# Optimization experiments

Hardware: AMD Instinct MI355X
Metric: run time of the kernel (lower is better)

Reference implementation:

```python
import jax, jax.numpy as jnp
from jax import lax
import numpy as np

ALPHA = 0.85   # TemporalSmoother alpha
EPS = 1e-5     # BatchNorm eps


def _bn(x, g, b):
    # eval-mode BatchNorm2d with running_mean=0, running_var=1 (fresh model)
    s = g / jnp.sqrt(1.0 + EPS)
    return x * s[None, :, None, None] + b[None, :, None, None]


def _conv(x, w, stride, pad):
    # x: NCHW (H=T, W=V), w: OIHW
    return lax.conv_general_dilated(x, w, window_strides=(stride, 1), padding=pad,
                                    dimension_numbers=('NCHW', 'OIHW', 'NCHW'))


def _block(x, A, gw, gb, g1, b1, tw, tb, g2, b2, rw, rb, stride):
    # residual 1x1 conv (always present: channels differ in every block)
    res = _conv(x, rw, stride, [(0, 0), (0, 0)]) + rb[None, :, None, None]
    # GraphConv: matmul(x, A.T) over joints, then 1x1 conv over channels
    h = jnp.einsum('nctv,wv->nctw', x, A)
    h = jnp.einsum('nctv,oc->notv', h, gw) + gb[None, :, None, None]
    # tcn: BN -> ReLU -> (9,1) conv stride (s,1) pad (4,0) -> BN
    h = jax.nn.relu(_bn(h, g1, b1))
    h = _conv(h, tw, stride, [(4, 4), (0, 0)]) + tb[None, :, None, None]
    h = _bn(h, g2, b2)
    return jax.nn.relu(h + res)


def _smooth(x):
    # EMA over time: s_t = a*s_{t-1} + (1-a)*x_t, s_0 = x_0 ; single lax.scan
    xt = jnp.moveaxis(x, 2, 0)  # (T, N, C, V)
    def step(s, xc):
        s = ALPHA * s + (1.0 - ALPHA) * xc
        return s, s
    _, ys = lax.scan(step, xt[0], xt[1:])
    return jnp.moveaxis(jnp.concatenate([xt[:1], ys], axis=0), 0, 2)


def setup_inputs() -> dict:
    key = jax.random.key(0)
    ks = jax.random.split(key, 12)
    N, C, T, V = 128, 2, 256, 18
    d = {}
    d['x'] = jax.random.normal(ks[0], (N, C, T, V), jnp.float32)
    d['A'] = jax.random.uniform(ks[1], (V, V), jnp.float32) / V  # normalized-ish adjacency
    d['dbn_g'] = jnp.ones((C * V,), jnp.float32)
    d['dbn_b'] = jnp.zeros((C * V,), jnp.float32)
    dims = [(2, 64), (64, 128), (128, 256)]
    for i, (ci, co) in enumerate(dims, 1):
        k = jax.random.split(ks[i + 1], 3)
        d[f'l{i}_gw'] = jax.random.normal(k[0], (co, ci), jnp.float32) * 0.1
        d[f'l{i}_gb'] = jnp.zeros((co,), jnp.float32)
        d[f'l{i}_bn1g'] = jnp.ones((co,), jnp.float32)
        d[f'l{i}_bn1b'] = jnp.zeros((co,), jnp.float32)
        d[f'l{i}_tw'] = jax.random.normal(k[1], (co, co, 9, 1), jnp.float32) * 0.05
        d[f'l{i}_tb'] = jnp.zeros((co,), jnp.float32)
        d[f'l{i}_bn2g'] = jnp.ones((co,), jnp.float32)
        d[f'l{i}_bn2b'] = jnp.zeros((co,), jnp.float32)
        d[f'l{i}_rw'] = jax.random.normal(k[2], (co, ci, 1, 1), jnp.float32) * 0.1
        d[f'l{i}_rb'] = jnp.zeros((co,), jnp.float32)
    d['fc_w'] = jax.random.normal(ks[10], (10, 256), jnp.float32) * 0.05
    d['fc_b'] = jnp.zeros((10,), jnp.float32)
    return d


def reference(x, A, dbn_g, dbn_b,
              l1_gw, l1_gb, l1_bn1g, l1_bn1b, l1_tw, l1_tb, l1_bn2g, l1_bn2b, l1_rw, l1_rb,
              l2_gw, l2_gb, l2_bn1g, l2_bn1b, l2_tw, l2_tb, l2_bn2g, l2_bn2b, l2_rw, l2_rb,
              l3_gw, l3_gb, l3_bn1g, l3_bn1b, l3_tw, l3_tb, l3_bn2g, l3_bn2b, l3_rw, l3_rb,
              fc_w, fc_b):
    N, C, T, V = x.shape
    # data_bn: BatchNorm1d over C*V features, eval mode (mean 0, var 1)
    xb = x.transpose(0, 1, 3, 2).reshape(N, C * V, T)
    s = dbn_g / jnp.sqrt(1.0 + EPS)
    xb = xb * s[None, :, None] + dbn_b[None, :, None]
    h = xb.reshape(N, C, V, T).transpose(0, 1, 3, 2)  # back to (N,C,T,V)
    h = _block(h, A, l1_gw, l1_gb, l1_bn1g, l1_bn1b, l1_tw, l1_tb, l1_bn2g, l1_bn2b, l1_rw, l1_rb, 1)
    h = _smooth(h)
    h = _block(h, A, l2_gw, l2_gb, l2_bn1g, l2_bn1b, l2_tw, l2_tb, l2_bn2g, l2_bn2b, l2_rw, l2_rb, 2)
    h = _smooth(h)
    h = _block(h, A, l3_gw, l3_gb, l3_bn1g, l3_bn1b, l3_tw, l3_tb, l3_bn2g, l3_bn2b, l3_rw, l3_rb, 2)
    h = _smooth(h)
    h = jnp.mean(h, axis=(2, 3))  # AdaptiveAvgPool2d((1,1))
    return h @ fc_w.T + fc_b
```

## Files before the change

### kernel.cpp

```cpp
#include <hip/hip_runtime.h>
#include <hip/hip_bf16.h>

#define EPS 1e-5f


typedef __attribute__((ext_vector_type(8))) short bf16x8;
typedef __attribute__((ext_vector_type(4))) float f32x4;
typedef __attribute__((ext_vector_type(4))) unsigned u32x4;

__device__ __forceinline__ unsigned short f2bf(float f) {
  unsigned u = __builtin_bit_cast(unsigned, f);
  u = (u + 0x7FFFu + ((u >> 16) & 1u)) >> 16;
  return (unsigned short)u;
}
__device__ __forceinline__ float bf2f(unsigned short h) {
  unsigned u = (unsigned)h << 16;
  return __builtin_bit_cast(float, u);
}


__global__ __launch_bounds__(256, 4) void k_transpose(
    const float* __restrict__ in, float* __restrict__ out, int rows, int cols) {
  int i = blockIdx.x * 256 + threadIdx.x;
  if (i < rows * cols) {
    int r = i / cols, c = i % cols;
    out[c * rows + r] = in[i];
  }
}

__global__ __launch_bounds__(256, 4) void k_beta(
    const float* __restrict__ bn2g, const float* __restrict__ bn2b,
    const float* __restrict__ tb, const float* __restrict__ rb,
    float* __restrict__ beta, int Co) {
  int o = blockIdx.x * 256 + threadIdx.x;
  if (o < Co)
    beta[o] = bn2g[o] * (1.0f / sqrtf(1.0f + EPS)) * tb[o] + bn2b[o] + rb[o];
}

__global__ __launch_bounds__(256, 4) void k_s1b1(
    const float* __restrict__ bn1g, const float* __restrict__ bn1b,
    const float* __restrict__ gb, float* __restrict__ s1v,
    float* __restrict__ b1p, int Co) {
  int o = blockIdx.x * 256 + threadIdx.x;
  if (o < Co) {
    float s1 = bn1g[o] * (1.0f / sqrtf(1.0f + EPS));
    s1v[o] = s1;
    b1p[o] = fmaf(s1, gb[o], bn1b[o]);
  }
}

__global__ __launch_bounds__(256, 4) void k_pack_conv9(
    const float* __restrict__ tw, const float* __restrict__ bn2g,
    unsigned short* __restrict__ out, int CO) {
  int KCc = CO / 32;
  int total = (CO / 16) * 9 * KCc * 512;
  int i = blockIdx.x * 256 + threadIdx.x;
  if (i >= total) return;
  int jj = i & 7, lane = (i >> 3) & 63, rest = i >> 9;
  int kc = rest % KCc; rest /= KCc;
  int j = rest % 9, ot = rest / 9;
  int q = lane >> 4, m = lane & 15;
  int c = kc * 32 + q * 8 + jj, o = ot * 16 + m;
  out[i] = f2bf(tw[((size_t)o * CO + c) * 9 + j] * bn2g[o] * (1.0f / sqrtf(1.0f + EPS)));
}

__global__ __launch_bounds__(256, 4) void k_pack_k32(
    const float* __restrict__ W, unsigned short* __restrict__ out, int K, int M) {
  int total = (M / 16) * (K / 32) * 512;
  int i = blockIdx.x * 256 + threadIdx.x;
  if (i >= total) return;
  int j = i & 7, lane = (i >> 3) & 63, rest = i >> 9;
  int kc = rest % (K / 32), ot = rest / (K / 32);
  int q = lane >> 4, m = lane & 15;
  int c = kc * 32 + q * 8 + j, o = ot * 16 + m;
  out[i] = f2bf(W[(size_t)o * K + c]);
}

__global__ __launch_bounds__(256, 4) void k_front1g(
    const float* __restrict__ x, const float* __restrict__ dbng,
    const float* __restrict__ dbnb, const float* __restrict__ Amat,
    const float* __restrict__ gw, const float* __restrict__ gb,
    const float* __restrict__ bn1g, const float* __restrict__ bn1b,
    unsigned short* __restrict__ Gt1, float* __restrict__ xb1) {
  int n = blockIdx.x, t0 = blockIdx.y * 64;
  __shared__ float xb[2304];
  __shared__ float xm[2304];
  __shared__ float As[324];
  __shared__ float g0s[64], g1s[64], bps[64];
  __shared__ unsigned short ldsT[64 * 65];
  const float rs = 1.0f / sqrtf(1.0f + EPS);
  for (int e = threadIdx.x; e < 324; e += 256) As[e] = Amat[e];
  if (threadIdx.x < 64) {
    int o = threadIdx.x;
    float s1 = bn1g[o] * rs;
    g0s[o] = gw[o * 2 + 0] * s1;
    g1s[o] = gw[o * 2 + 1] * s1;
    bps[o] = fmaf(s1, gb[o], bn1b[o]);
  }
  for (int e = threadIdx.x; e < 2304; e += 256) {
    int c = e / 1152, r = e % 1152;
    int v = r % 18;
    xb[e] = x[(n * 2 + c) * 4608 + t0 * 18 + r] * (dbng[c * 18 + v] * rs) + dbnb[c * 18 + v];
  }
  __syncthreads();
  for (int e = threadIdx.x; e < 2304; e += 256) {
    int c = e / 1152, r = e % 1152;
    int v = r / 64, tt = r % 64;
    xb1[((size_t)(n * 2 + c) * 18 + v) * 256 + t0 + tt] = xb[c * 1152 + tt * 18 + v];
  }
  for (int e = threadIdx.x; e < 2304; e += 256) {
    int c = e / 1152, r = e % 1152;
    int tt = r / 18, v = r % 18;
    const float* xr = &xb[c * 1152 + tt * 18];
    float z = 0.0f;
#pragma unroll
    for (int w = 0; w < 18; w++) z = fmaf(As[v * 18 + w], xr[w], z);
    xm[e] = z;
  }
  __syncthreads();
  for (int v = 0; v < 18; v++) {
    for (int e = threadIdx.x; e < 4096; e += 256) {
      int o = e >> 6, tt = e & 63;
      float z = fmaf(g0s[o], xm[tt * 18 + v], fmaf(g1s[o], xm[1152 + tt * 18 + v], bps[o]));
      z = z > 0.0f ? z : 0.0f;
      ldsT[o * 65 + tt] = f2bf(z);
    }
    __syncthreads();
    for (int e = threadIdx.x; e < 4096; e += 256) {
      int tt = e >> 6, o = e & 63;
      Gt1[((size_t)(n * 18 + v) * 272 + 8 + t0 + tt) * 64 + o] = ldsT[o * 65 + tt];
    }
    __syncthreads();
  }
  if (blockIdx.y == 0 || blockIdx.y == 3) {
    int base = (blockIdx.y == 0) ? 0 : 264;
    for (int e = threadIdx.x; e < 18 * 8 * 64; e += 256) {
      int v = e / 512, r = e % 512;
      int tg = base + (r >> 6), o = r & 63;
      Gt1[((size_t)(n * 18 + v) * 272 + tg) * 64 + o] = 0;
    }
  }
}

template <int CO, int T>
__global__ __launch_bounds__(256, 4) void k_amixX(
    const unsigned short* __restrict__ Xt, unsigned short* __restrict__ Xm,
    const float* __restrict__ Amat) {
  int idx = blockIdx.x * 256 + threadIdx.x;
  int c = idx & (CO - 1);
  int t = (idx / CO) & (T - 1);
  int n = idx / (CO * T);
  const size_t stride = (size_t)T * CO;
  const unsigned short* bp = Xt + (size_t)n * 18 * stride + (size_t)t * CO + c;
  unsigned short* op = Xm + (size_t)n * 18 * stride + (size_t)t * CO + c;
  float xs[18];
#pragma unroll
  for (int w = 0; w < 18; w++) xs[w] = bf2f(bp[w * stride]);
#pragma unroll
  for (int v = 0; v < 18; v++) {
    float z = 0.0f;
#pragma unroll
    for (int w = 0; w < 18; w++) z = fmaf(Amat[v * 18 + w], xs[w], z);
    op[v * stride] = f2bf(z);
  }
}

template <int CI, int CO, int TIN>
__global__ __launch_bounds__(64, 4) void k_ugemmG(
    const unsigned short* __restrict__ Xm, const unsigned short* __restrict__ Ag,
    const float* __restrict__ s1v, const float* __restrict__ b1p,
    unsigned short* __restrict__ Gt) {
  constexpr int NP = 18 * TIN;
  constexpr int Trr = TIN + 16;
  const int n = blockIdx.x;
  const int p0 = blockIdx.y * 32;
  const int otg = blockIdx.z;
  const int lane = threadIdx.x;
  const int q = lane >> 4, nn = lane & 15;
  constexpr int KC = CI / 32;
  const int v = p0 / TIN;
  const int tb = p0 % TIN;
  __shared__ unsigned short ldsT[32 * 36];
  f32x4 acc[2][2] = {};
  const unsigned short* Xn = Xm + (size_t)n * NP * CI;
  for (int kc = 0; kc < KC; kc++) {
    bf16x8 A[2];
#pragma unroll
    for (int i = 0; i < 2; i++)
      A[i] = *(const bf16x8*)(Ag + (((size_t)(otg * 2 + i) * KC + kc) * 64 + lane) * 8);
#pragma unroll
    for (int u = 0; u < 2; u++) {
      bf16x8 B = *(const bf16x8*)(Xn + (size_t)(p0 + u * 16 + nn) * CI + kc * 32 + q * 8);
#pragma unroll
      for (int i = 0; i < 2; i++)
        acc[i][u] = __builtin_amdgcn_mfma_f32_16x16x32_bf16(A[i], B, acc[i][u], 0, 0, 0);
    }
  }
#pragma unroll
  for (int i = 0; i < 2; i++) {
    int obl = i * 16 + q * 4;
    int ob = otg * 32 + obl;
    const float4 s4 = *(const float4*)&s1v[ob];
    const float4 b4 = *(const float4*)&b1p[ob];
#pragma unroll
    for (int u = 0; u < 2; u++) {
      unsigned short zb[4];
#pragma unroll
      for (int r = 0; r < 4; r++) {
        float z = fmaf(acc[i][u][r], ((const float*)&s4)[r], ((const float*)&b4)[r]);
        z = z > 0.0f ? z : 0.0f;
        zb[r] = f2bf(z);
      }
      *(unsigned long long*)&ldsT[(u * 16 + nn) * 36 + obl] =
          *(const unsigned long long*)zb;
    }
  }
  __syncthreads();
  for (int e = lane; e < 1024; e += 64) {
    int tq = e >> 5, cq2 = e & 31;
    Gt[((size_t)(n * 18 + v) * Trr + 8 + tb + tq) * CO + otg * 32 + cq2] = ldsT[tq * 36 + cq2];
  }
  if (tb == 0) {
    for (int g = 0; g < 8; g++) {
      int idx = g * 64 + lane;
      int r16 = idx >> 5, c = otg * 32 + (idx & 31);
      int tg = (r16 < 8) ? r16 : (TIN + r16);
      Gt[((size_t)(n * 18 + v) * Trr + tg) * CO + c] = 0;
    }
  }
}

template <int CIN, int CO, int S, int TIN, int TOUT, int OTB, int TB>
__global__ __launch_bounds__(64 * (CO / (16 * OTB)) < 256 ? 64 * (CO / (16 * OTB)) : 256, 3)
void k_conv(
    const unsigned short* __restrict__ Gt, const unsigned short* __restrict__ Xt,
    const float* __restrict__ XB, const unsigned short* __restrict__ Aj,
    const unsigned short* __restrict__ Ar, const float* __restrict__ rwT1,
    const float* __restrict__ beta, unsigned short* __restrict__ Out) {
  static_assert(TB == 2, "NT formula assumes 32 to's per block");
  constexpr int Trr = TIN + 16;
  constexpr int WAVES = CO / (16 * OTB);
  constexpr int THREADS = 64 * WAVES;
  constexpr int KCc = CO / 32;
  constexpr int NT = (S == 2) ? 72 : 40;
  constexpr int NP = (NT * 2 * CO * 2 > 49152) ? 2 : 1;
  constexpr int CP = CO / NP;
  constexpr int KCP = CP / 32;
  constexpr int LKCP = (KCP == 4) ? 2 : 1;
  constexpr int M9 = 9 * KCP;
  constexpr int KCR = (CIN >= 32) ? CIN / 32 : 0;

  const int n = blockIdx.x;
  const int to_base = blockIdx.y * (16 * TB);
  const int v0 = blockIdx.z * 2;
  const int otg = threadIdx.x >> 6;
  const int lane = threadIdx.x & 63;
  const int q = lane >> 4, nn = lane & 15;
  const int ti0 = S * to_base - 4;

  __shared__ unsigned short Bs[NT * 2 * CP];

  f32x4 acc[OTB][TB][2] = {};

  unsigned linb[TB][2];
  int tla[TB];
#pragma unroll
  for (int tb = 0; tb < TB; tb++) {
    int t0 = S * (tb * 16 + nn);
    tla[tb] = t0;
#pragma unroll
    for (int u = 0; u < 2; u++)
      linb[tb][u] = (unsigned)(((u * NT + t0) * CP + q * 8) * 2);
  }

  const unsigned short* Acp = Aj + (size_t)lane * 8;

  auto loadA = [&](int m, int ph, bf16x8 (&A)[OTB]) {
    int j = m >> LKCP, kcg = ph * KCP + (m & (KCP - 1));
#pragma unroll
    for (int i = 0; i < OTB; i++)
      A[i] = *(const bf16x8*)(Acp +
          (((size_t)(otg * OTB + i) * 9 + j) * KCc + kcg) * 512);
  };
  auto loadB = [&](int m, bf16x8 (&B)[TB][2]) {
    int j = m >> LKCP, kcl = m & (KCP - 1);
    unsigned joff = (unsigned)j * (unsigned)(CP * 2) + (unsigned)kcl * 64u;
#pragma unroll
    for (int tb = 0; tb < TB; tb++) {
      unsigned swz = ((((unsigned)(tla[tb] + j)) >> 1) & 7u) << 4;
#pragma unroll
      for (int u = 0; u < 2; u++) {
        unsigned byte = (linb[tb][u] + joff) ^ swz;
        B[tb][u] = *(const bf16x8*)((const char*)Bs + byte);
      }
    }
  };
  auto mfmaB = [&](bf16x8 (&A)[OTB], bf16x8 (&B)[TB][2]) {
#pragma unroll
    for (int i = 0; i < OTB; i++)
#pragma unroll
      for (int tb = 0; tb < TB; tb++)
#pragma unroll
        for (int u = 0; u < 2; u++)
          acc[i][tb][u] =
              __builtin_amdgcn_mfma_f32_16x16x32_bf16(A[i], B[tb][u], acc[i][tb][u],
                                                      0, 0, 0);
  };

#pragma unroll 1
  for (int ph = 0; ph < NP; ph++) {
    constexpr int CPC = CP / 8;
    constexpr int TOTCH = NT * 2 * CPC;
    for (int e = (int)threadIdx.x; e < TOTCH; e += THREADS) {
      int cc = e % CPC, rest = e / CPC;
      int u = rest & 1, tl = rest >> 1;
      const unsigned short* src = Gt +
          ((size_t)(n * 18 + v0 + u) * Trr + (size_t)(8 + ti0 + tl)) * CO +
          ph * CP + cc * 8;
      u32x4 d = *(const u32x4*)src;
      unsigned hb = (((unsigned)(u * NT + tl) * CP + (unsigned)cc * 8u) * 2u) ^
                    ((((unsigned)tl >> 1) & 7u) << 4);
      *(u32x4*)((char*)Bs + hb) = d;
    }
    __syncthreads();

    bf16x8 Aa[OTB], Ba[TB][2], Ab[OTB], Bb[TB][2];
    loadA(0, ph, Aa); loadB(0, Ba);
    loadA(1, ph, Ab); loadB(1, Bb);
#pragma unroll 1
    for (int m = 0; m < M9; m += 2) {
      mfmaB(Aa, Ba);
      if (m + 2 < M9) { loadA(m + 2, ph, Aa); loadB(m + 2, Ba); }
      __builtin_amdgcn_sched_barrier(0);
      mfmaB(Ab, Bb);
      if (m + 3 < M9) { loadA(m + 3, ph, Ab); loadB(m + 3, Bb); }
      __builtin_amdgcn_sched_barrier(0);
    }
    if (ph + 1 < NP) __syncthreads();
  }

  if constexpr (CIN >= 32) {
    unsigned r_tu[TB][2];
#pragma unroll
    for (int tb = 0; tb < TB; tb++)
#pragma unroll
      for (int u = 0; u < 2; u++) {
        int t = S * (to_base + tb * 16 + nn);
        r_tu[tb][u] = (unsigned)(((n * 18 + v0 + u) * TIN + t) * CIN + q * 8);
      }
    auto loadAr = [&](int kcr, bf16x8 (&A)[OTB]) {
#pragma unroll
      for (int i = 0; i < OTB; i++)
        A[i] = *(const bf16x8*)(Ar + (((size_t)(otg * OTB + i) * KCR + kcr) * 64 + lane) * 8);
    };
    auto loadBr = [&](int kcr, bf16x8 (&B)[TB][2]) {
#pragma unroll
      for (int tb = 0; tb < TB; tb++)
#pragma unroll
        for (int u = 0; u < 2; u++)
          B[tb][u] = *(const bf16x8*)(Xt + r_tu[tb][u] + (unsigned)kcr * 32u);
    };
    bf16x8 Ra[OTB], Sa[TB][2], Rb[OTB], Sb[TB][2];
    loadAr(0, Ra); loadBr(0, Sa);
    loadAr(1, Rb); loadBr(1, Sb);
#pragma unroll 1
    for (int kcr = 0; kcr < KCR; kcr += 2) {
      mfmaB(Ra, Sa);
      if (kcr + 2 < KCR) { loadAr(kcr + 2, Ra); loadBr(kcr + 2, Sa); }
      __builtin_amdgcn_sched_barrier(0);
      mfmaB(Rb, Sb);
      if (kcr + 3 < KCR) { loadAr(kcr + 3, Rb); loadBr(kcr + 3, Sb); }
      __builtin_amdgcn_sched_barrier(0);
    }
  } else {
#pragma unroll
    for (int ci = 0; ci < 2; ci++) {
#pragma unroll
      for (int tb = 0; tb < TB; tb++)
#pragma unroll
        for (int u = 0; u < 2; u++) {
          float xv =
              XB[(((size_t)n * 2 + ci) * 18 + v0 + u) * TIN + S * (to_base + tb * 16 + nn)];
#pragma unroll
          for (int i = 0; i < OTB; i++) {
            const float4 w4 = *(const float4*)&rwT1[ci * CO + (otg * OTB + i) * 16 + q * 4];
            acc[i][tb][u][0] = fmaf(w4.x, xv, acc[i][tb][u][0]);
            acc[i][tb][u][1] = fmaf(w4.y, xv, acc[i][tb][u][1]);
            acc[i][tb][u][2] = fmaf(w4.z, xv, acc[i][tb][u][2]);
            acc[i][tb][u][3] = fmaf(w4.w, xv, acc[i][tb][u][3]);
          }
        }
    }
  }

#pragma unroll
  for (int i = 0; i < OTB; i++) {
    int ob = (otg * OTB + i) * 16 + q * 4;
    const float4 bt = *(const float4*)&beta[ob];
#pragma unroll
    for (int tb = 0; tb < TB; tb++)
#pragma unroll
      for (int u = 0; u < 2; u++) {
        int v = v0 + u, to = to_base + tb * 16 + nn;
#pragma unroll
        for (int r = 0; r < 4; r++) {
          float val = acc[i][tb][u][r] + ((const float*)&bt)[r];
          Out[(((size_t)n * CO + ob + r) * 18 + v) * TOUT + to] =
              f2bf(val > 0.0f ? val : 0.0f);
        }
      }
  }
}

__global__ __launch_bounds__(64) void k_smooth2(
    const unsigned short* __restrict__ X, unsigned short* __restrict__ Xt,
    int CO, int T) {
  __shared__ float tile[64 * 33];
  int n = blockIdx.x, v = blockIdx.y, c0 = blockIdx.z * 64;
  int tid = threadIdx.x;
  float s = 0.0f;
  for (int tc = 0; tc < T; tc += 32) {
    for (int e = tid; e < 64 * 32; e += 64) {
      int cc = e >> 5, tt = e & 31;
      tile[cc * 33 + tt] = bf2f(X[((size_t)(n * CO + c0 + cc) * 18 + v) * T + tc + tt]);
    }
    __syncthreads();
    float* row = &tile[tid * 33];
    int start = 0;
    if (tc == 0) { s = row[0]; start = 1; }
    for (int tt = start; tt < 32; tt++) {
      s = fmaf(0.85f, s, 0.15f * row[tt]);
      row[tt] = s;
    }
    for (int it = 0; it < 32; it++)
      Xt[((size_t)(n * 18 + v) * T + tc + it) * CO + c0 + tid] = f2bf(tile[tid * 33 + it]);
    __syncthreads();
  }
}

__global__ __launch_bounds__(64) void k_smooth(unsigned short* __restrict__ X, int T) {
  __shared__ float tile[64 * 33];
  size_t r0 = (size_t)blockIdx.x * 64;
  float s = 0.0f;
  for (int tc = 0; tc < T; tc += 32) {
    for (int e = threadIdx.x; e < 64 * 32; e += 64) {
      int r = e >> 5, tt = e & 31;
      tile[r * 33 + tt] = bf2f(X[(r0 + r) * T + tc + tt]);
    }
    __syncthreads();
    float* row = &tile[threadIdx.x * 33];
    int start = 0;
    if (tc == 0) { s = row[0]; start = 1; }
    for (int tt = start; tt < 32; tt++) {
      s = fmaf(0.85f, s, 0.15f * row[tt]);
      row[tt] = s;
    }
    __syncthreads();
    for (int e = threadIdx.x; e < 64 * 32; e += 64) {
      int r = e >> 5, tt = e & 31;
      X[(r0 + r) * T + tc + tt] = f2bf(tile[r * 33 + tt]);
    }
    __syncthreads();
  }
}

__global__ __launch_bounds__(256, 4) void k_poolfc(
    const unsigned short* __restrict__ H, const float* __restrict__ fcw,
    const float* __restrict__ fcb, float* __restrict__ out) {
  int n = blockIdx.x;
  __shared__ float pool[256];
  const unsigned short* row = H + (size_t)(n * 256 + threadIdx.x) * 1152;
  float s = 0.0f;
  for (int i = 0; i < 1152; i += 8) {
    u32x4 d = *(const u32x4*)(row + i);
#pragma unroll
    for (int k = 0; k < 4; k++) {
      unsigned dv = ((const unsigned*)&d)[k];
      s += __builtin_bit_cast(float, dv << 16);
      s += __builtin_bit_cast(float, dv & 0xFFFF0000u);
    }
  }
  pool[threadIdx.x] = s * (1.0f / 1152.0f);
  __syncthreads();
  if (threadIdx.x < 10) {
    float a = fcb[threadIdx.x];
    for (int c = 0; c < 256; c++) a = fmaf(fcw[threadIdx.x * 256 + c], pool[c], a);
    out[n * 10 + threadIdx.x] = a;
  }
}

extern "C" void kernel_launch(void* const* d_in, const int* in_sizes, int n_in,
                              void* d_out, int out_size, void* d_ws, size_t ws_size,
                              hipStream_t stream) {
  const float* x    = (const float*)d_in[0];
  const float* Amat = (const float*)d_in[1];
  const float* dbng = (const float*)d_in[2];
  const float* dbnb = (const float*)d_in[3];
  const float* gw1 = (const float*)d_in[4];   const float* gb1 = (const float*)d_in[5];
  const float* bn1g1 = (const float*)d_in[6]; const float* bn1b1 = (const float*)d_in[7];
  const float* tw1 = (const float*)d_in[8];   const float* tb1 = (const float*)d_in[9];
  const float* bn2g1 = (const float*)d_in[10]; const float* bn2b1 = (const float*)d_in[11];
  const float* rw1 = (const float*)d_in[12];  const float* rb1 = (const float*)d_in[13];
  const float* gw2 = (const float*)d_in[14];  const float* gb2 = (const float*)d_in[15];
  const float* bn1g2 = (const float*)d_in[16]; const float* bn1b2 = (const float*)d_in[17];
  const float* tw2 = (const float*)d_in[18];  const float* tb2 = (const float*)d_in[19];
  const float* bn2g2 = (const float*)d_in[20]; const float* bn2b2 = (const float*)d_in[21];
  const float* rw2 = (const float*)d_in[22];  const float* rb2 = (const float*)d_in[23];
  const float* gw3 = (const float*)d_in[24];  const float* gb3 = (const float*)d_in[25];
  const float* bn1g3 = (const float*)d_in[26]; const float* bn1b3 = (const float*)d_in[27];
  const float* tw3 = (const float*)d_in[28];  const float* tb3 = (const float*)d_in[29];
  const float* bn2g3 = (const float*)d_in[30]; const float* bn2b3 = (const float*)d_in[31];
  const float* rw3 = (const float*)d_in[32];  const float* rb3 = (const float*)d_in[33];
  const float* fcw = (const float*)d_in[34];  const float* fcb = (const float*)d_in[35];
  (void)in_sizes; (void)n_in; (void)out_size;

  float* f = (float*)d_ws;
  float* rwT1  = f;
  float* beta1 = rwT1 + 128;
  float* beta2 = beta1 + 64;
  float* beta3 = beta2 + 128;
  float* s1v2  = beta3 + 256;
  float* b1p2  = s1v2 + 128;
  float* s1v3  = b1p2 + 128;
  float* b1p3  = s1v3 + 256;
  unsigned short* H = (unsigned short*)(f + 2048);
  unsigned short* Aj1 = H;
  unsigned short* Aj2 = Aj1 + 36864;
  unsigned short* Aj3 = Aj2 + 147456;
  unsigned short* Ar2 = Aj3 + 589824;
  unsigned short* Ar3 = Ar2 + 8192;
  unsigned short* Ag2 = Ar3 + 32768;
  unsigned short* Ag3 = Ag2 + 8192;
  const size_t WOFFB = 8192 + 856064ULL * 2;

  const size_t PERN = 3723264ULL;
  long long avail = (long long)ws_size - (long long)WOFFB - 256;
  int NC = (avail > 0) ? (int)(avail / (long long)PERN) : 1;
  if (NC > 64) NC = 64;
  if (NC < 1) NC = 1;
  {
    int nch = (128 + NC - 1) / NC;
    NC = (128 + nch - 1) / nch;
  }
  char* wb = (char*)d_ws;
  unsigned short* B1 = (unsigned short*)(wb + WOFFB);
  unsigned short* B2 = B1 + (size_t)NC * 294912;
  float* XB = (float*)((char*)B2 + (size_t)NC * 589824);
  unsigned short* Gt = (unsigned short*)((char*)XB + (size_t)NC * 36864);
  unsigned short* Xt = (unsigned short*)((char*)Gt + (size_t)NC * 1327104);
  unsigned short* Xm = Xt + (size_t)NC * 294912;

  k_transpose<<<1, 256, 0, stream>>>(rw1, rwT1, 64, 2);
  k_beta<<<1, 256, 0, stream>>>(bn2g1, bn2b1, tb1, rb1, beta1, 64);
  k_beta<<<1, 256, 0, stream>>>(bn2g2, bn2b2, tb2, rb2, beta2, 128);
  k_beta<<<1, 256, 0, stream>>>(bn2g3, bn2b3, tb3, rb3, beta3, 256);
  k_s1b1<<<1, 256, 0, stream>>>(bn1g2, bn1b2, gb2, s1v2, b1p2, 128);
  k_s1b1<<<1, 256, 0, stream>>>(bn1g3, bn1b3, gb3, s1v3, b1p3, 256);
  k_pack_conv9<<<144, 256, 0, stream>>>(tw1, bn2g1, Aj1, 64);
  k_pack_conv9<<<576, 256, 0, stream>>>(tw2, bn2g2, Aj2, 128);
  k_pack_conv9<<<2304, 256, 0, stream>>>(tw3, bn2g3, Aj3, 256);
  k_pack_k32<<<32, 256, 0, stream>>>(rw2, Ar2, 64, 128);
  k_pack_k32<<<128, 256, 0, stream>>>(rw3, Ar3, 128, 256);
  k_pack_k32<<<32, 256, 0, stream>>>(gw2, Ag2, 64, 128);
  k_pack_k32<<<128, 256, 0, stream>>>(gw3, Ag3, 128, 256);

  for (int n0 = 0; n0 < 128; n0 += NC) {
    const int nc = (128 - n0 < NC) ? 128 - n0 : NC;
    k_front1g<<<dim3(nc, 4), 256, 0, stream>>>(
        x + (size_t)n0 * 9216, dbng, dbnb, Amat, gw1, gb1, bn1g1, bn1b1, Gt, XB);
    k_conv<2, 64, 1, 256, 256, 4, 2><<<dim3(nc, 8, 9), 64, 0, stream>>>(
        Gt, nullptr, XB, Aj1, nullptr, rwT1, beta1, B1);
    k_smooth2<<<dim3(nc, 18, 1), 64, 0, stream>>>(B1, Xt, 64, 256);
    k_amixX<64, 256><<<nc * 64, 256, 0, stream>>>(Xt, Xm, Amat);
    k_ugemmG<64, 128, 256><<<dim3(nc, 144, 4), 64, 0, stream>>>(
        Xm, Ag2, s1v2, b1p2, Gt);
    k_conv<64, 128, 2, 256, 128, 4, 2><<<dim3(nc, 4, 9), 128, 0, stream>>>(
        Gt, Xt, nullptr, Aj2, Ar2, nullptr, beta2, B2);
    k_smooth2<<<dim3(nc, 18, 2), 64, 0, stream>>>(B2, Xt, 128, 128);
    k_amixX<128, 128><<<nc * 64, 256, 0, stream>>>(Xt, Xm, Amat);
    k_ugemmG<128, 256, 128><<<dim3(nc, 72, 8), 64, 0, stream>>>(
        Xm, Ag3, s1v3, b1p3, Gt);
    k_conv<128, 256, 2, 128, 64, 4, 2><<<dim3(nc, 2, 9), 256, 0, stream>>>(
        Gt, Xt, nullptr, Aj3, Ar3, nullptr, beta3, B1);
    k_smooth<<<nc * 72, 64, 0, stream>>>(B1, 64);
    k_poolfc<<<nc, 256, 0, stream>>>(B1, fcw, fcb, (float*)d_out + (size_t)n0 * 10);
  }
}
```

Before: 1.156 ms.

## Enlarge conv wave tile to 64 time steps and stage channels in 64-wide phases

Doubles the per-wave temporal tile in the temporal conv kernel from 32 to 64 outputs (TB=4), halving the grid's time dimension. Shared-memory staging now always uses 64-channel phases with a fixed 18-step K loop. The A-fragment loads are hoisted before the barrier, and B fragments are loaded from LDS just before each MFMA group instead of being double-buffered. The aim is more weight reuse per LDS tile and fewer redundant halo loads, at the cost of higher register pressure (launch-bounds occupancy lowered from 3 to 2) and fewer blocks.

```diff
diff --git a/kernel.cpp b/kernel.cpp
--- a/kernel.cpp
+++ b/kernel.cpp
@@ -231,27 +231,25 @@
 }
 
 template <int CIN, int CO, int S, int TIN, int TOUT, int OTB, int TB>
-__global__ __launch_bounds__(64 * (CO / (16 * OTB)) < 256 ? 64 * (CO / (16 * OTB)) : 256, 3)
+__global__ __launch_bounds__(64 * (CO / (16 * OTB)) < 256 ? 64 * (CO / (16 * OTB)) : 256, 2)
 void k_conv(
     const unsigned short* __restrict__ Gt, const unsigned short* __restrict__ Xt,
     const float* __restrict__ XB, const unsigned short* __restrict__ Aj,
     const unsigned short* __restrict__ Ar, const float* __restrict__ rwT1,
     const float* __restrict__ beta, unsigned short* __restrict__ Out) {
-  static_assert(TB == 2, "NT formula assumes 32 to's per block");
+  static_assert(TB == 4 && OTB == 4, "geometry assumes 64t x 64o per wave");
   constexpr int Trr = TIN + 16;
   constexpr int WAVES = CO / (16 * OTB);
   constexpr int THREADS = 64 * WAVES;
   constexpr int KCc = CO / 32;
-  constexpr int NT = (S == 2) ? 72 : 40;
-  constexpr int NP = (NT * 2 * CO * 2 > 49152) ? 2 : 1;
-  constexpr int CP = CO / NP;
-  constexpr int KCP = CP / 32;
-  constexpr int LKCP = (KCP == 4) ? 2 : 1;
-  constexpr int M9 = 9 * KCP;
+  constexpr int NT = S * 64 + 8;
+  constexpr int CP = 64;
+  constexpr int NP = CO / CP;
+  constexpr int M9 = 18;
   constexpr int KCR = (CIN >= 32) ? CIN / 32 : 0;
 
   const int n = blockIdx.x;
-  const int to_base = blockIdx.y * (16 * TB);
+  const int to_base = blockIdx.y * 64;
   const int v0 = blockIdx.z * 2;
   const int otg = threadIdx.x >> 6;
   const int lane = threadIdx.x & 63;
@@ -276,14 +274,14 @@
   const unsigned short* Acp = Aj + (size_t)lane * 8;
 
   auto loadA = [&](int m, int ph, bf16x8 (&A)[OTB]) {
-    int j = m >> LKCP, kcg = ph * KCP + (m & (KCP - 1));
+    int j = m >> 1, kcg = ph * 2 + (m & 1);
 #pragma unroll
     for (int i = 0; i < OTB; i++)
       A[i] = *(const bf16x8*)(Acp +
           (((size_t)(otg * OTB + i) * 9 + j) * KCc + kcg) * 512);
   };
   auto loadB = [&](int m, bf16x8 (&B)[TB][2]) {
-    int j = m >> LKCP, kcl = m & (KCP - 1);
+    int j = m >> 1, kcl = m & 1;
     unsigned joff = (unsigned)j * (unsigned)(CP * 2) + (unsigned)kcl * 64u;
 #pragma unroll
     for (int tb = 0; tb < TB; tb++) {
@@ -312,7 +310,7 @@
     constexpr int CPC = CP / 8;
     constexpr int TOTCH = NT * 2 * CPC;
     for (int e = (int)threadIdx.x; e < TOTCH; e += THREADS) {
-      int cc = e % CPC, rest = e / CPC;
+      int cc = e & 7, rest = e >> 3;
       int u = rest & 1, tl = rest >> 1;
       const unsigned short* src = Gt +
           ((size_t)(n * 18 + v0 + u) * Trr + (size_t)(8 + ti0 + tl)) * CO +
@@ -322,18 +320,26 @@
                     ((((unsigned)tl >> 1) & 7u) << 4);
       *(u32x4*)((char*)Bs + hb) = d;
     }
-    __syncthreads();
-
-    bf16x8 Aa[OTB], Ba[TB][2], Ab[OTB], Bb[TB][2];
-    loadA(0, ph, Aa); loadB(0, Ba);
-    loadA(1, ph, Ab); loadB(1, Bb);
+    bf16x8 Aa[OTB], Ab[OTB];
+    loadA(0, ph, Aa);
+    loadA(1, ph, Ab);
+    __syncthreads();
+
 #pragma unroll 1
     for (int m = 0; m < M9; m += 2) {
-      mfmaB(Aa, Ba);
-      if (m + 2 < M9) { loadA(m + 2, ph, Aa); loadB(m + 2, Ba); }
+      {
+        bf16x8 B[TB][2];
+        loadB(m, B);
+        mfmaB(Aa, B);
+      }
+      if (m + 2 < M9) loadA(m + 2, ph, Aa);
       __builtin_amdgcn_sched_barrier(0);
-      mfmaB(Ab, Bb);
-      if (m + 3 < M9) { loadA(m + 3, ph, Ab); loadB(m + 3, Bb); }
+      {
+        bf16x8 B[TB][2];
+        loadB(m + 1, B);
+        mfmaB(Ab, B);
+      }
+      if (m + 3 < M9) loadA(m + 3, ph, Ab);
       __builtin_amdgcn_sched_barrier(0);
     }
     if (ph + 1 < NP) __syncthreads();
@@ -568,19 +574,19 @@
     const int nc = (128 - n0 < NC) ? 128 - n0 : NC;
     k_front1g<<<dim3(nc, 4), 256, 0, stream>>>(
         x + (size_t)n0 * 9216, dbng, dbnb, Amat, gw1, gb1, bn1g1, bn1b1, Gt, XB);
-    k_conv<2, 64, 1, 256, 256, 4, 2><<<dim3(nc, 8, 9), 64, 0, stream>>>(
+    k_conv<2, 64, 1, 256, 256, 4, 4><<<dim3(nc, 4, 9), 64, 0, stream>>>(
         Gt, nullptr, XB, Aj1, nullptr, rwT1, beta1, B1);
     k_smooth2<<<dim3(nc, 18, 1), 64, 0, stream>>>(B1, Xt, 64, 256);
     k_amixX<64, 256><<<nc * 64, 256, 0, stream>>>(Xt, Xm, Amat);
     k_ugemmG<64, 128, 256><<<dim3(nc, 144, 4), 64, 0, stream>>>(
         Xm, Ag2, s1v2, b1p2, Gt);
-    k_conv<64, 128, 2, 256, 128, 4, 2><<<dim3(nc, 4, 9), 128, 0, stream>>>(
+    k_conv<64, 128, 2, 256, 128, 4, 4><<<dim3(nc, 2, 9), 128, 0, stream>>>(
         Gt, Xt, nullptr, Aj2, Ar2, nullptr, beta2, B2);
     k_smooth2<<<dim3(nc, 18, 2), 64, 0, stream>>>(B2, Xt, 128, 128);
     k_amixX<128, 128><<<nc * 64, 256, 0, stream>>>(Xt, Xm, Amat);
     k_ugemmG<128, 256, 128><<<dim3(nc, 72, 8), 64, 0, stream>>>(
         Xm, Ag3, s1v3, b1p3, Gt);
-    k_conv<128, 256, 2, 128, 64, 4, 2><<<dim3(nc, 2, 9), 256, 0, stream>>>(
+    k_conv<128, 256, 2, 128, 64, 4, 4><<<dim3(nc, 1, 9), 256, 0, stream>>>(
         Gt, Xt, nullptr, Aj3, Ar3, nullptr, beta3, B1);
     k_smooth<<<nc * 72, 64, 0, stream>>>(B1, 64);
     k_poolfc<<<nc, 256, 0, stream>>>(B1, fcw, fcb, (float*)d_out + (size_t)n0 * 10);
```

New measurement: 1.164 ms. No clear change (+0.7%).
